# Kernel optimization log

Hardware: AMD Instinct MI355X
Metric: run time of the kernel (lower is better)

## Reference

```python
import jax, jax.numpy as jnp
import numpy as np

N = 100000      # nodes
E = 3200000     # edges (avg degree 32)
F_IN = 32       # n_features
H = 64          # GCN hidden width


def setup_inputs() -> dict:
    key = jax.random.key(0)
    ks = jax.random.split(key, 14)
    x = jax.random.normal(ks[0], (N, F_IN), jnp.float32)
    edge_index = jax.random.randint(ks[1], (2, E), 0, N, dtype=jnp.int32)
    labels = jax.random.bernoulli(ks[2], 0.1, (N, 1)).astype(jnp.float32)

    def lin(k, fan_in, fan_out):
        kw, kb = jax.random.split(k)
        bound = 1.0 / np.sqrt(fan_in)
        W = jax.random.uniform(kw, (fan_in, fan_out), jnp.float32, -bound, bound)
        b = jax.random.uniform(kb, (fan_out,), jnp.float32, -bound, bound)
        return W, b

    W1, b1 = lin(ks[3], F_IN, H)
    W2, b2 = lin(ks[4], H, H)
    W3, b3 = lin(ks[5], H, H)
    Wl1, bl1 = lin(ks[6], H, 8)
    Wl2, bl2 = lin(ks[7], 8, 1)
    return dict(x=x, edge_index=edge_index, labels=labels,
                W1=W1, b1=b1, W2=W2, b2=b2, W3=W3, b3=b3,
                Wl1=Wl1, bl1=bl1, Wl2=Wl2, bl2=bl2)


def _gcn(h, row, col, norm_edge, deg_inv, W, b):
    # GCNConv: D^{-1/2} (A + I) D^{-1/2} (h W) + b, with added self-loops.
    m = h @ W                                   # [N, out]
    msg = m[row] * norm_edge[:, None]           # [E, out] gather + scale
    agg = jax.ops.segment_sum(msg, col, num_segments=N)
    agg = agg + m * deg_inv[:, None]            # self-loop term: deg^{-1/2}_i * deg^{-1/2}_i
    return agg + b


def reference(x, edge_index, labels, W1, b1, W2, b2, W3, b3, Wl1, bl1, Wl2, bl2):
    row, col = edge_index[0], edge_index[1]
    # degree with self-loops (counts incoming edges at target nodes)
    deg = jax.ops.segment_sum(jnp.ones((E,), jnp.float32), col, num_segments=N) + 1.0
    deg_isqrt = jax.lax.rsqrt(deg)
    norm_edge = deg_isqrt[row] * deg_isqrt[col]  # [E]
    deg_inv = deg_isqrt * deg_isqrt              # self-loop norm = 1/deg

    h = jax.nn.relu(_gcn(x, row, col, norm_edge, deg_inv, W1, b1))
    # dropout is identity in eval mode
    h = jax.nn.relu(_gcn(h, row, col, norm_edge, deg_inv, W2, b2))
    h = jax.nn.relu(_gcn(h, row, col, norm_edge, deg_inv, W3, b3))
    h = jax.nn.relu(h @ Wl1 + bl1)
    z = h @ Wl2 + bl2                            # [N, 1]
    p = jax.nn.sigmoid(z)

    # generate_weights(labels): class-balanced weights
    n_pos = jnp.sum(labels)
    n_tot = jnp.float32(labels.size)
    w_pos = n_tot / (2.0 * n_pos)
    w_neg = n_tot / (2.0 * (n_tot - n_pos))
    w = labels * w_pos + (1.0 - labels) * w_neg

    # stable BCE on logits (equivalent to binary_cross_entropy(sigmoid(z), y))
    bce = -(labels * jax.nn.log_sigmoid(z) + (1.0 - labels) * jax.nn.log_sigmoid(-z))
    loss = jnp.mean(w * bce)
    return (loss, p)
```

## Files before the change

### kernel.cpp

```cpp
#include <hip/hip_runtime.h>
#include <math.h>

#define N_NODES 100000
#define N_EDGES 3200000
#define NPB 256
#define NBUCK ((N_NODES + NPB - 1) / NPB)
#define NPW 4

typedef unsigned short ushort_t;

static __device__ __forceinline__ float bf2f(ushort_t u) {
    return __uint_as_float(((unsigned int)u) << 16);
}
static __device__ __forceinline__ unsigned int f2bf_u(float f) {
    unsigned int x = __float_as_uint(f);
    unsigned int lsb = (x >> 16) & 1u;
    x += 0x7fffu + lsb;
    return x >> 16;
}
static __device__ __forceinline__ ushort_t f2bf(float f) { return (ushort_t)f2bf_u(f); }

__global__ void bucket_hist_kernel(const int* __restrict__ col, int* __restrict__ bucketCnt) {
    __shared__ int h[NBUCK];
    for (int t = threadIdx.x; t < NBUCK; t += 256) h[t] = 0;
    __syncthreads();
    for (int e = blockIdx.x * 256 + threadIdx.x; e < N_EDGES; e += gridDim.x * 256)
        atomicAdd(&h[col[e] >> 8], 1);
    __syncthreads();
    for (int t = threadIdx.x; t < NBUCK; t += 256)
        if (h[t]) atomicAdd(&bucketCnt[t], h[t]);
}

__global__ void bucket_scan_kernel(const int* __restrict__ bucketCnt, int* __restrict__ bucketOff,
                                   int* __restrict__ bcursor) {
    __shared__ int tmp[512];
    int tx = threadIdx.x;
    int v = (tx < NBUCK) ? bucketCnt[tx] : 0;
    tmp[tx] = v;
    __syncthreads();
    for (int off = 1; off < 512; off <<= 1) {
        int t = (tx >= off) ? tmp[tx - off] : 0;
        __syncthreads();
        if (tx >= off) tmp[tx] += t;
        __syncthreads();
    }
    if (tx < NBUCK) {
        int o = tmp[tx] - v;
        bucketOff[tx] = o;
        bcursor[tx] = o;
    }
}

__global__ void bin_kernel(const int* __restrict__ row, const int* __restrict__ col,
                           int* __restrict__ bcursor, int2* __restrict__ tmpE) {
    __shared__ int hist[NBUCK];
    __shared__ int chunkOff[NBUCK];
    int tx = threadIdx.x;
    for (int t = tx; t < NBUCK; t += 512) hist[t] = 0;
    __syncthreads();
    int base = blockIdx.x * 4096;
    int myc[8], myr[8], myrank[8];
#pragma unroll 8
    for (int k = 0; k < 8; ++k) {
        int idx = base + k * 512 + tx;
        bool valid = idx < N_EDGES;
        int c = valid ? col[idx] : 0;
        int r = valid ? row[idx] : 0;
        myc[k] = c;
        myr[k] = r;
        myrank[k] = valid ? atomicAdd(&hist[c >> 8], 1) : 0;
    }
    __syncthreads();
    for (int t = tx; t < NBUCK; t += 512) {
        int hv = hist[t];
        chunkOff[t] = hv ? atomicAdd(&bcursor[t], hv) : 0;
    }
    __syncthreads();
#pragma unroll 8
    for (int k = 0; k < 8; ++k) {
        int idx = base + k * 512 + tx;
        if (idx < N_EDGES) {
            int pos = chunkOff[myc[k] >> 8] + myrank[k];
            tmpE[pos] = make_int2(myr[k], myc[k]);
        }
    }
}

__global__ void csr_kernel(const int2* __restrict__ tmpE, const int* __restrict__ bucketOff,
                           const int* __restrict__ bucketCnt, int* __restrict__ starts,
                           int* __restrict__ edgeRow, float* __restrict__ isq,
                           const float* __restrict__ labels, float* __restrict__ npos) {
    __shared__ int scnt[NPB];
    __shared__ int sscan[NPB];
    __shared__ int scur[NPB];
    __shared__ float red[NPB];
    int b = blockIdx.x;
    int lo = b * NPB;
    int nn = N_NODES - lo;
    if (nn > NPB) nn = NPB;
    int base = bucketOff[b];
    int ecnt = bucketCnt[b];
    int tx = threadIdx.x;
    scnt[tx] = 0;
    __syncthreads();
    for (int t = tx; t < ecnt; t += NPB) atomicAdd(&scnt[tmpE[base + t].y - lo], 1);
    __syncthreads();
    int v = scnt[tx];
    sscan[tx] = v;
    __syncthreads();
    for (int off = 1; off < NPB; off <<= 1) {
        int t = (tx >= off) ? sscan[tx - off] : 0;
        __syncthreads();
        if (tx >= off) sscan[tx] += t;
        __syncthreads();
    }
    int excl = sscan[tx] - v;
    scur[tx] = excl;
    float lab = 0.0f;
    if (tx < nn) {
        starts[lo + tx] = base + excl;
        isq[lo + tx] = rsqrtf((float)v + 1.0f);
        lab = labels[lo + tx];
    }
    if (b == NBUCK - 1 && tx == 0) starts[N_NODES] = N_EDGES;
    red[tx] = lab;
    __syncthreads();
    for (int s = NPB / 2; s > 0; s >>= 1) {
        if (tx < s) red[tx] += red[tx + s];
        __syncthreads();
    }
    if (tx == 0) atomicAdd(npos, red[0]);
    for (int t = tx; t < ecnt; t += NPB) {
        int2 rc = tmpE[base + t];
        int p = atomicAdd(&scur[rc.y - lo], 1);
        edgeRow[base + p] = rc.x;
    }
}

__global__ void norm_fill_kernel(const int* __restrict__ starts, const int* __restrict__ edgeRow,
                                 const float* __restrict__ isq, int2* __restrict__ edgeRN) {
    int w = threadIdx.x >> 6;
    int lane = threadIdx.x & 63;
    int nodeBase = blockIdx.x * (4 * NPW) + w * NPW;
    for (int i = 0; i < NPW; ++i) {
        int node = nodeBase + i;
        int s = starts[node];
        int e = starts[node + 1];
        float si = isq[node];
        for (int t = s + lane; t < e; t += 64) {
            int r = edgeRow[t];
            edgeRN[t] = make_int2(r, __float_as_int(isq[r] * si));
        }
    }
}

__global__ void xcast_kernel(const float* __restrict__ x, ushort_t* __restrict__ xbf) {
    int i = blockIdx.x * 256 + threadIdx.x;
    if (i < (N_NODES * 32) / 4) {
        float4 v = ((const float4*)x)[i];
        ushort4 o;
        o.x = f2bf(v.x); o.y = f2bf(v.y); o.z = f2bf(v.z); o.w = f2bf(v.w);
        ((ushort4*)xbf)[i] = o;
    }
}

__global__ void wpack_kernel(const float* __restrict__ W1, const float* __restrict__ W2,
                             const float* __restrict__ W3, unsigned int* __restrict__ wp) {
    int t = blockIdx.x * 256 + threadIdx.x;
    if (t >= 80 * 64) return;
    int k2 = t >> 6, l = t & 63;
    const float* W;
    int kk;
    if (k2 < 16) { W = W1; kk = k2; }
    else if (k2 < 48) { W = W2; kk = k2 - 16; }
    else { W = W3; kk = k2 - 48; }
    float lo = W[(2 * kk) * 64 + l];
    float hi = W[(2 * kk + 1) * 64 + l];
    wp[t] = (f2bf_u(hi) << 16) | f2bf_u(lo);
}

__global__ void fused32_kernel(const int* __restrict__ starts, const int2* __restrict__ edgeRN,
                               const ushort_t* __restrict__ xbf, const float* __restrict__ isq,
                               const unsigned int* __restrict__ wpG,
                               const float* __restrict__ bias, ushort_t* __restrict__ hout) {
    __shared__ float sAgg[4][32];
    int w = threadIdx.x >> 6;
    int lane = threadIdx.x & 63;
    int f = lane & 31, half = lane >> 5;
    unsigned int wpk[16];
#pragma unroll
    for (int k2 = 0; k2 < 16; ++k2) wpk[k2] = wpG[k2 * 64 + lane];
    float bias_r = bias[lane];
    int nodeBase = blockIdx.x * (4 * NPW) + w * NPW;
    for (int i = 0; i < NPW; ++i) {
        int node = __builtin_amdgcn_readfirstlane(nodeBase + i);
        int sU = starts[node];
        int eU = starts[node + 1];
        float si = isq[node];
        float acc[4] = {0.0f, 0.0f, 0.0f, 0.0f};
        int j = sU;
        for (; j + 8 <= eU; j += 8) {
            int2 rn[8];
#pragma unroll
            for (int q = 0; q < 8; ++q) rn[q] = edgeRN[j + q];
            unsigned int vv[8];
#pragma unroll
            for (int q = 0; q < 8; ++q) {
                const ushort_t* rowp = xbf + (rn[q].x << 5);
                vv[q] = rowp[f];
            }
#pragma unroll
            for (int q = 0; q < 8; ++q)
                acc[q & 3] = fmaf(bf2f((ushort_t)vv[q]), __int_as_float(rn[q].y), acc[q & 3]);
        }
        for (; j < eU; ++j) {
            int2 rn = edgeRN[j];
            const ushort_t* rowp = xbf + (rn.x << 5);
            acc[0] = fmaf(bf2f(rowp[f]), __int_as_float(rn.y), acc[0]);
        }
        float accsum = (acc[0] + acc[1]) + (acc[2] + acc[3]);
        if (half == 0) {
            accsum = fmaf(bf2f(xbf[(node << 5) + f]), si * si, accsum);
            sAgg[w][f] = accsum;
        }
        float o = bias_r;
#pragma unroll
        for (int q = 0; q < 8; ++q) {
            float4 av = *(const float4*)&sAgg[w][q * 4];
            unsigned int p0 = wpk[2 * q], p1 = wpk[2 * q + 1];
            o = fmaf(av.x, __uint_as_float(p0 << 16), o);
            o = fmaf(av.y, __uint_as_float(p0 & 0xffff0000u), o);
            o = fmaf(av.z, __uint_as_float(p1 << 16), o);
            o = fmaf(av.w, __uint_as_float(p1 & 0xffff0000u), o);
        }
        o = o > 0.0f ? o : 0.0f;
        hout[(node << 6) + lane] = f2bf(o);
    }
}

__global__ void fused64_kernel(const int* __restrict__ starts, const int2* __restrict__ edgeRN,
                               const ushort_t* __restrict__ hin, const float* __restrict__ isq,
                               const unsigned int* __restrict__ wpG,
                               const float* __restrict__ bias, ushort_t* __restrict__ hout) {
    __shared__ float sAgg[4][64];
    int w = threadIdx.x >> 6;
    int lane = threadIdx.x & 63;
    unsigned int wpk[32];
#pragma unroll
    for (int k2 = 0; k2 < 32; ++k2) wpk[k2] = wpG[k2 * 64 + lane];
    float bias_r = bias[lane];
    int nodeBase = blockIdx.x * (4 * NPW) + w * NPW;
    for (int i = 0; i < NPW; ++i) {
        int node = __builtin_amdgcn_readfirstlane(nodeBase + i);
        int sU = starts[node];
        int eU = starts[node + 1];
        float si = isq[node];
        float acc[4];
        acc[0] = bf2f(hin[(node << 6) + lane]) * (si * si);
        acc[1] = 0.0f; acc[2] = 0.0f; acc[3] = 0.0f;
        int j = sU;
        for (; j + 8 <= eU; j += 8) {
            int2 rn[8];
#pragma unroll
            for (int q = 0; q < 8; ++q) rn[q] = edgeRN[j + q];
            unsigned int vv[8];
#pragma unroll
            for (int q = 0; q < 8; ++q) {
                const ushort_t* rowp = hin + (rn[q].x << 6);
                vv[q] = rowp[lane];
            }
#pragma unroll
            for (int q = 0; q < 8; ++q)
                acc[q & 3] = fmaf(bf2f((ushort_t)vv[q]), __int_as_float(rn[q].y), acc[q & 3]);
        }
        for (; j < eU; ++j) {
            int2 rn = edgeRN[j];
            const ushort_t* rowp = hin + (rn.x << 6);
            acc[0] = fmaf(bf2f(rowp[lane]), __int_as_float(rn.y), acc[0]);
        }
        sAgg[w][lane] = (acc[0] + acc[1]) + (acc[2] + acc[3]);
        float o = bias_r;
#pragma unroll
        for (int q = 0; q < 16; ++q) {
            float4 av = *(const float4*)&sAgg[w][q * 4];
            unsigned int p0 = wpk[2 * q], p1 = wpk[2 * q + 1];
            o = fmaf(av.x, __uint_as_float(p0 << 16), o);
            o = fmaf(av.y, __uint_as_float(p0 & 0xffff0000u), o);
            o = fmaf(av.z, __uint_as_float(p1 << 16), o);
            o = fmaf(av.w, __uint_as_float(p1 & 0xffff0000u), o);
        }
        o = o > 0.0f ? o : 0.0f;
        hout[(node << 6) + lane] = f2bf(o);
    }
}

__global__ void head_kernel(const ushort_t* __restrict__ h, const float* __restrict__ Wl1,
                            const float* __restrict__ bl1, const float* __restrict__ Wl2,
                            const float* __restrict__ bl2, const float* __restrict__ labels,
                            const float* __restrict__ npos, float* __restrict__ out) {
    __shared__ float sW1[64 * 8];
    __shared__ float sb1[8];
    __shared__ float sW2[8];
    for (int t = threadIdx.x; t < 512; t += 256) sW1[t] = Wl1[t];
    if (threadIdx.x < 8) {
        sb1[threadIdx.x] = bl1[threadIdx.x];
        sW2[threadIdx.x] = Wl2[threadIdx.x];
    }
    __syncthreads();
    int i = blockIdx.x * 256 + threadIdx.x;
    float contrib = 0.0f;
    if (i < N_NODES) {
        const ushort4* hr4 = (const ushort4*)(h + (size_t)i * 64);
        float a[8];
#pragma unroll
        for (int j = 0; j < 8; ++j) a[j] = sb1[j];
#pragma unroll
        for (int kb = 0; kb < 16; ++kb) {
            ushort4 v4 = hr4[kb];
            float h0 = bf2f(v4.x), h1 = bf2f(v4.y), h2 = bf2f(v4.z), h3 = bf2f(v4.w);
#pragma unroll
            for (int j = 0; j < 8; ++j) {
                a[j] = fmaf(h0, sW1[(kb * 4 + 0) * 8 + j], a[j]);
                a[j] = fmaf(h1, sW1[(kb * 4 + 1) * 8 + j], a[j]);
                a[j] = fmaf(h2, sW1[(kb * 4 + 2) * 8 + j], a[j]);
                a[j] = fmaf(h3, sW1[(kb * 4 + 3) * 8 + j], a[j]);
            }
        }
        float z = bl2[0];
#pragma unroll
        for (int j = 0; j < 8; ++j) {
            float r = a[j] > 0.0f ? a[j] : 0.0f;
            z = fmaf(r, sW2[j], z);
        }
        float p = 1.0f / (1.0f + expf(-z));
        out[1 + i] = p;
        float y = labels[i];
        float np = *npos;
        float fn = (float)N_NODES;
        float wpos = fn / (2.0f * np);
        float wneg = fn / (2.0f * (fn - np));
        float wgt = y * wpos + (1.0f - y) * wneg;
        float lse = log1pf(expf(-fabsf(z)));
        float ls_pos = fminf(z, 0.0f) - lse;
        float ls_neg = fminf(-z, 0.0f) - lse;
        float bce = -(y * ls_pos + (1.0f - y) * ls_neg);
        contrib = wgt * bce / fn;
    }
    __shared__ float red[256];
    red[threadIdx.x] = contrib;
    __syncthreads();
    for (int s = 128; s > 0; s >>= 1) {
        if (threadIdx.x < s) red[threadIdx.x] += red[threadIdx.x + s];
        __syncthreads();
    }
    if (threadIdx.x == 0) atomicAdd(out, red[0]);
}

extern "C" void kernel_launch(void* const* d_in, const int* in_sizes, int n_in,
                              void* d_out, int out_size, void* d_ws, size_t ws_size,
                              hipStream_t stream) {
    const float* x      = (const float*)d_in[0];
    const int*   ei     = (const int*)d_in[1];
    const float* labels = (const float*)d_in[2];
    const float* W1  = (const float*)d_in[3];
    const float* b1  = (const float*)d_in[4];
    const float* W2  = (const float*)d_in[5];
    const float* b2  = (const float*)d_in[6];
    const float* W3  = (const float*)d_in[7];
    const float* b3  = (const float*)d_in[8];
    const float* Wl1 = (const float*)d_in[9];
    const float* bl1 = (const float*)d_in[10];
    const float* Wl2 = (const float*)d_in[11];
    const float* bl2 = (const float*)d_in[12];

    const int* row = ei;
    const int* col = ei + N_EDGES;
    float* out = (float*)d_out;

    char* w = (char*)d_ws;
    int2*     tmpE    = (int2*)w;
    int2*     edgeRN  = (int2*)w;
    int*      edgeRow = (int*)(w + (size_t)N_EDGES * 8);
    ushort_t* xbf     = (ushort_t*)(edgeRow + N_EDGES);
    ushort_t* hbfA    = xbf + (size_t)N_NODES * 32;
    ushort_t* hbfB    = hbfA + (size_t)N_NODES * 64;
    int*      starts  = (int*)(hbfB + (size_t)N_NODES * 64);
    int*      bucketCnt = starts + (N_NODES + 1);
    int*      bucketOff = bucketCnt + NBUCK;
    int*      bcursor   = bucketOff + NBUCK;
    float*    isq  = (float*)(bcursor + NBUCK);
    float*    npos = isq + N_NODES;
    unsigned int* wpG = (unsigned int*)(npos + 1);

    hipMemsetAsync(bucketCnt, 0, NBUCK * sizeof(int), stream);
    hipMemsetAsync(npos, 0, sizeof(float), stream);
    hipMemsetAsync(out, 0, sizeof(float), stream);

    const int FB = N_NODES / (4 * NPW);
    const int BB = (N_EDGES + 4095) / 4096;
    const int XB = (N_NODES * 32 / 4 + 255) / 256;

    bucket_hist_kernel<<<1024, 256, 0, stream>>>(col, bucketCnt);
    bucket_scan_kernel<<<1, 512, 0, stream>>>(bucketCnt, bucketOff, bcursor);
    bin_kernel<<<BB, 512, 0, stream>>>(row, col, bcursor, tmpE);
    csr_kernel<<<NBUCK, NPB, 0, stream>>>(tmpE, bucketOff, bucketCnt, starts, edgeRow, isq,
                                          labels, npos);
    norm_fill_kernel<<<FB, 256, 0, stream>>>(starts, edgeRow, isq, edgeRN);
    xcast_kernel<<<XB, 256, 0, stream>>>(x, xbf);
    wpack_kernel<<<20, 256, 0, stream>>>(W1, W2, W3, wpG);

    fused32_kernel<<<FB, 256, 0, stream>>>(starts, edgeRN, xbf, isq, wpG, b1, hbfA);
    fused64_kernel<<<FB, 256, 0, stream>>>(starts, edgeRN, hbfA, isq, wpG + 16 * 64, b2, hbfB);
    fused64_kernel<<<FB, 256, 0, stream>>>(starts, edgeRN, hbfB, isq, wpG + 48 * 64, b3, hbfA);

    head_kernel<<<(N_NODES + 255) / 256, 256, 0, stream>>>(hbfA, Wl1, bl1, Wl2, bl2, labels,
                                                           npos, out);
}
```

Before: 435.4 us.

## Fold symmetric degree normalization into node features and drop per-edge norm array

Pre-scales node features by deg^-1/2 (in the cast kernel and each layer's output) so aggregation becomes a plain sum over neighbors, scaled by the target's deg^-1/2 afterward. This removes the norm_fill kernel and the 8-byte int2 edge stream, letting the gather kernels read only 4-byte row indices. The edge loop is also restructured into padded groups of 16 with masking, which needs a zeroed tail pad after edgeRow. The cost is an extra bf16 rounding of the scaled activations and wasted loads on partial groups.

```diff
diff --git a/kernel.cpp b/kernel.cpp
--- a/kernel.cpp
+++ b/kernel.cpp
@@ -137,30 +137,15 @@
     }
 }
 
-__global__ void norm_fill_kernel(const int* __restrict__ starts, const int* __restrict__ edgeRow,
-                                 const float* __restrict__ isq, int2* __restrict__ edgeRN) {
-    int w = threadIdx.x >> 6;
-    int lane = threadIdx.x & 63;
-    int nodeBase = blockIdx.x * (4 * NPW) + w * NPW;
-    for (int i = 0; i < NPW; ++i) {
-        int node = nodeBase + i;
-        int s = starts[node];
-        int e = starts[node + 1];
-        float si = isq[node];
-        for (int t = s + lane; t < e; t += 64) {
-            int r = edgeRow[t];
-            edgeRN[t] = make_int2(r, __float_as_int(isq[r] * si));
-        }
-    }
-}
-
-__global__ void xcast_kernel(const float* __restrict__ x, ushort_t* __restrict__ xbf) {
+__global__ void xcast_kernel(const float* __restrict__ x, const float* __restrict__ isq,
+                             ushort_t* __restrict__ xs) {
     int i = blockIdx.x * 256 + threadIdx.x;
     if (i < (N_NODES * 32) / 4) {
+        float s = isq[i >> 3];
         float4 v = ((const float4*)x)[i];
         ushort4 o;
-        o.x = f2bf(v.x); o.y = f2bf(v.y); o.z = f2bf(v.z); o.w = f2bf(v.w);
-        ((ushort4*)xbf)[i] = o;
+        o.x = f2bf(v.x * s); o.y = f2bf(v.y * s); o.z = f2bf(v.z * s); o.w = f2bf(v.w * s);
+        ((ushort4*)xs)[i] = o;
     }
 }
 
@@ -179,8 +164,8 @@
     wp[t] = (f2bf_u(hi) << 16) | f2bf_u(lo);
 }
 
-__global__ void fused32_kernel(const int* __restrict__ starts, const int2* __restrict__ edgeRN,
-                               const ushort_t* __restrict__ xbf, const float* __restrict__ isq,
+__global__ void fused32_kernel(const int* __restrict__ starts, const int* __restrict__ edgeRow,
+                               const ushort_t* __restrict__ xs, const float* __restrict__ isq,
                                const unsigned int* __restrict__ wpG,
                                const float* __restrict__ bias, ushort_t* __restrict__ hout) {
     __shared__ float sAgg[4][32];
@@ -196,32 +181,28 @@
         int node = __builtin_amdgcn_readfirstlane(nodeBase + i);
         int sU = starts[node];
         int eU = starts[node + 1];
-        float si = isq[node];
+        float sic = isq[node];
         float acc[4] = {0.0f, 0.0f, 0.0f, 0.0f};
-        int j = sU;
-        for (; j + 8 <= eU; j += 8) {
-            int2 rn[8];
-#pragma unroll
-            for (int q = 0; q < 8; ++q) rn[q] = edgeRN[j + q];
-            unsigned int vv[8];
-#pragma unroll
-            for (int q = 0; q < 8; ++q) {
-                const ushort_t* rowp = xbf + (rn[q].x << 5);
-                vv[q] = rowp[f];
+        int ngrp = (eU - sU + 15) >> 4;
+        int jb = sU;
+        for (int g = 0; g < ngrp; ++g) {
+            int rows[16];
+#pragma unroll
+            for (int q = 0; q < 16; ++q) rows[q] = edgeRow[jb + q];
+            unsigned int vv[16];
+#pragma unroll
+            for (int q = 0; q < 16; ++q) vv[q] = xs[(rows[q] << 5) + f];
+#pragma unroll
+            for (int q = 0; q < 16; ++q) {
+                float n = (jb + q < eU) ? 1.0f : 0.0f;
+                acc[q & 3] = fmaf(bf2f((ushort_t)vv[q]), n, acc[q & 3]);
             }
-#pragma unroll
-            for (int q = 0; q < 8; ++q)
-                acc[q & 3] = fmaf(bf2f((ushort_t)vv[q]), __int_as_float(rn[q].y), acc[q & 3]);
-        }
-        for (; j < eU; ++j) {
-            int2 rn = edgeRN[j];
-            const ushort_t* rowp = xbf + (rn.x << 5);
-            acc[0] = fmaf(bf2f(rowp[f]), __int_as_float(rn.y), acc[0]);
+            jb += 16;
         }
         float accsum = (acc[0] + acc[1]) + (acc[2] + acc[3]);
         if (half == 0) {
-            accsum = fmaf(bf2f(xbf[(node << 5) + f]), si * si, accsum);
-            sAgg[w][f] = accsum;
+            accsum += bf2f(xs[(node << 5) + f]);
+            sAgg[w][f] = accsum * sic;
         }
         float o = bias_r;
 #pragma unroll
@@ -234,14 +215,15 @@
             o = fmaf(av.w, __uint_as_float(p1 & 0xffff0000u), o);
         }
         o = o > 0.0f ? o : 0.0f;
-        hout[(node << 6) + lane] = f2bf(o);
-    }
-}
-
-__global__ void fused64_kernel(const int* __restrict__ starts, const int2* __restrict__ edgeRN,
-                               const ushort_t* __restrict__ hin, const float* __restrict__ isq,
+        hout[(node << 6) + lane] = f2bf(o * sic);
+    }
+}
+
+__global__ void fused64_kernel(const int* __restrict__ starts, const int* __restrict__ edgeRow,
+                               const ushort_t* __restrict__ hs, const float* __restrict__ isq,
                                const unsigned int* __restrict__ wpG,
-                               const float* __restrict__ bias, ushort_t* __restrict__ hout) {
+                               const float* __restrict__ bias, ushort_t* __restrict__ hout,
+                               int outScaled) {
     __shared__ float sAgg[4][64];
     int w = threadIdx.x >> 6;
     int lane = threadIdx.x & 63;
@@ -254,31 +236,27 @@
         int node = __builtin_amdgcn_readfirstlane(nodeBase + i);
         int sU = starts[node];
         int eU = starts[node + 1];
-        float si = isq[node];
+        float sic = isq[node];
         float acc[4];
-        acc[0] = bf2f(hin[(node << 6) + lane]) * (si * si);
+        acc[0] = bf2f(hs[(node << 6) + lane]);
         acc[1] = 0.0f; acc[2] = 0.0f; acc[3] = 0.0f;
-        int j = sU;
-        for (; j + 8 <= eU; j += 8) {
-            int2 rn[8];
-#pragma unroll
-            for (int q = 0; q < 8; ++q) rn[q] = edgeRN[j + q];
-            unsigned int vv[8];
-#pragma unroll
-            for (int q = 0; q < 8; ++q) {
-                const ushort_t* rowp = hin + (rn[q].x << 6);
-                vv[q] = rowp[lane];
+        int ngrp = (eU - sU + 15) >> 4;
+        int jb = sU;
+        for (int g = 0; g < ngrp; ++g) {
+            int rows[16];
+#pragma unroll
+            for (int q = 0; q < 16; ++q) rows[q] = edgeRow[jb + q];
+            unsigned int vv[16];
+#pragma unroll
+            for (int q = 0; q < 16; ++q) vv[q] = hs[(rows[q] << 6) + lane];
+#pragma unroll
+            for (int q = 0; q < 16; ++q) {
+                float n = (jb + q < eU) ? 1.0f : 0.0f;
+                acc[q & 3] = fmaf(bf2f((ushort_t)vv[q]), n, acc[q & 3]);
             }
-#pragma unroll
-            for (int q = 0; q < 8; ++q)
-                acc[q & 3] = fmaf(bf2f((ushort_t)vv[q]), __int_as_float(rn[q].y), acc[q & 3]);
-        }
-        for (; j < eU; ++j) {
-            int2 rn = edgeRN[j];
-            const ushort_t* rowp = hin + (rn.x << 6);
-            acc[0] = fmaf(bf2f(rowp[lane]), __int_as_float(rn.y), acc[0]);
-        }
-        sAgg[w][lane] = (acc[0] + acc[1]) + (acc[2] + acc[3]);
+            jb += 16;
+        }
+        sAgg[w][lane] = ((acc[0] + acc[1]) + (acc[2] + acc[3])) * sic;
         float o = bias_r;
 #pragma unroll
         for (int q = 0; q < 16; ++q) {
@@ -290,7 +268,8 @@
             o = fmaf(av.w, __uint_as_float(p1 & 0xffff0000u), o);
         }
         o = o > 0.0f ? o : 0.0f;
-        hout[(node << 6) + lane] = f2bf(o);
+        float scale = outScaled ? sic : 1.0f;
+        hout[(node << 6) + lane] = f2bf(o * scale);
     }
 }
 
@@ -379,9 +358,8 @@
 
     char* w = (char*)d_ws;
     int2*     tmpE    = (int2*)w;
-    int2*     edgeRN  = (int2*)w;
     int*      edgeRow = (int*)(w + (size_t)N_EDGES * 8);
-    ushort_t* xbf     = (ushort_t*)(edgeRow + N_EDGES);
+    ushort_t* xbf     = (ushort_t*)(edgeRow + N_EDGES + 16);
     ushort_t* hbfA    = xbf + (size_t)N_NODES * 32;
     ushort_t* hbfB    = hbfA + (size_t)N_NODES * 64;
     int*      starts  = (int*)(hbfB + (size_t)N_NODES * 64);
@@ -395,6 +373,7 @@
     hipMemsetAsync(bucketCnt, 0, NBUCK * sizeof(int), stream);
     hipMemsetAsync(npos, 0, sizeof(float), stream);
     hipMemsetAsync(out, 0, sizeof(float), stream);
+    hipMemsetAsync(edgeRow + N_EDGES, 0, 16 * sizeof(int), stream);
 
     const int FB = N_NODES / (4 * NPW);
     const int BB = (N_EDGES + 4095) / 4096;
@@ -405,13 +384,14 @@
     bin_kernel<<<BB, 512, 0, stream>>>(row, col, bcursor, tmpE);
     csr_kernel<<<NBUCK, NPB, 0, stream>>>(tmpE, bucketOff, bucketCnt, starts, edgeRow, isq,
                                           labels, npos);
-    norm_fill_kernel<<<FB, 256, 0, stream>>>(starts, edgeRow, isq, edgeRN);
-    xcast_kernel<<<XB, 256, 0, stream>>>(x, xbf);
+    xcast_kernel<<<XB, 256, 0, stream>>>(x, isq, xbf);
     wpack_kernel<<<20, 256, 0, stream>>>(W1, W2, W3, wpG);
 
-    fused32_kernel<<<FB, 256, 0, stream>>>(starts, edgeRN, xbf, isq, wpG, b1, hbfA);
-    fused64_kernel<<<FB, 256, 0, stream>>>(starts, edgeRN, hbfA, isq, wpG + 16 * 64, b2, hbfB);
-    fused64_kernel<<<FB, 256, 0, stream>>>(starts, edgeRN, hbfB, isq, wpG + 48 * 64, b3, hbfA);
+    fused32_kernel<<<FB, 256, 0, stream>>>(starts, edgeRow, xbf, isq, wpG, b1, hbfA);
+    fused64_kernel<<<FB, 256, 0, stream>>>(starts, edgeRow, hbfA, isq, wpG + 16 * 64, b2,
+                                           hbfB, 1);
+    fused64_kernel<<<FB, 256, 0, stream>>>(starts, edgeRow, hbfB, isq, wpG + 48 * 64, b3,
+                                           hbfA, 0);
 
     head_kernel<<<(N_NODES + 255) / 256, 256, 0, stream>>>(hbfA, Wl1, bl1, Wl2, bl2, labels,
                                                            npos, out);
```

After: 415.3 us. -4.6%, faster.
